# Optimization experiments

Measured on AMD Instinct MI355X. Metric: run time of the kernel, lower is better.

Reference implementation:

```python
import jax, jax.numpy as jnp
import numpy as np

B = 4096          # batch
N_ENT = 200000    # n_entities
N_USR = 50000
N_REL = 32
K = 64            # neighbors per entity
D2 = 128          # dim*2
EPS = 1e-5


def setup_inputs() -> dict:
    key = jax.random.key(0)
    ks = jax.random.split(key, 10)
    return {
        "u": jax.random.randint(ks[0], (B,), 0, N_USR),
        "i": jax.random.randint(ks[1], (B,), 0, N_ENT),
        "adj_entity": jax.random.randint(ks[2], (N_ENT, K), 0, N_ENT),
        "adj_relation": jax.random.randint(ks[3], (N_ENT, K), 0, N_REL),
        "entity_embs": jax.random.normal(ks[4], (N_ENT, D2), jnp.float32),
        "relation_embs": jax.random.normal(ks[5], (N_REL, D2), jnp.float32),
        "bn_gamma": jnp.ones((D2,), jnp.float32),
        "bn_beta": jnp.zeros((D2,), jnp.float32),
        "bn_mean": jnp.zeros((D2,), jnp.float32),
        "bn_var": jnp.ones((D2,), jnp.float32),
        "Wr1_w": jax.random.normal(ks[6], (D2, D2), jnp.float32) * 0.05,
        "Wr1_b": jnp.zeros((D2,), jnp.float32),
        "W1_w": jax.random.normal(ks[7], (D2, D2), jnp.float32) * 0.05,
        "W1_b": jnp.zeros((D2,), jnp.float32),
        "wl_w": jax.random.normal(ks[8], (2 * D2, 1), jnp.float32) * 0.05,
        "wl_b": jnp.zeros((1,), jnp.float32),
    }


def reference(u, i, adj_entity, adj_relation, entity_embs, relation_embs,
              bn_gamma, bn_beta, bn_mean, bn_var,
              Wr1_w, Wr1_b, W1_w, W1_b, wl_w, wl_b):
    # eval mode: all dropout / edge-drop are identity, BN uses running stats
    def bn(x):
        return (x - bn_mean) * bn_gamma * jax.lax.rsqrt(bn_var + EPS) + bn_beta

    def lrelu(x):
        return jnp.where(x >= 0, x, 0.2 * x)

    def layer(h, idx):
        t = entity_embs[adj_entity[idx]]        # [B, K, D2] neighbor gather
        r = relation_embs[adj_relation[idx]]    # [B, K, D2]
        tr = t @ Wr1_w + Wr1_b                  # Wr1(t)
        hr = jnp.tanh((h @ Wr1_w + Wr1_b)[:, None, :] + r)
        hrt = hr * tr                           # [B, K, D2]
        s = jnp.sum(hrt, axis=1)
        Nh = s * s - jnp.sum(hrt * hrt, axis=1)  # FM: sq-of-sum - sum-of-sq
        out = lrelu((h + Nh) @ W1_w + W1_b)      # agg_method='other'
        return h + out

    u_e = bn(entity_embs[u])
    h = bn(entity_embs[i])
    # n_layers = 1
    h = layer(h, i)
    u_e = layer(u_e, u)
    combined = jnp.concatenate([u_e, h], axis=-1)  # [B, 2*D2]
    return (combined @ wl_w + wl_b)[:, 0]
```

## Files before the change

kernel.cpp:

```cpp
#include <hip/hip_runtime.h>

#define B     4096
#define KNB   64
#define D     128
#define NREL  32
#define EPS   1e-5f

typedef __attribute__((ext_vector_type(8))) short bf16x8;
typedef __attribute__((ext_vector_type(4))) float f32x4;

__device__ inline unsigned short f2bf(float f) {
    unsigned u = __float_as_uint(f);
    return (unsigned short)((u + 0x7FFFu + ((u >> 16) & 1u)) >> 16);
}
__device__ inline unsigned cvt_pk_bf16(float lo, float hi) {
    unsigned r;
    asm("v_cvt_pk_bf16_f32 %0, %1, %2" : "=v"(r) : "v"(lo), "v"(hi));
    return r;
}
__device__ inline unsigned short cvt1_bf16(float f) {
    return (unsigned short)(cvt_pk_bf16(f, f) & 0xFFFFu);
}
__device__ inline float bfu_lo(unsigned u) { return __uint_as_float(u << 16); }
__device__ inline float bfu_hi(unsigned u) { return __uint_as_float(u & 0xFFFF0000u); }

__device__ inline float fast_tanh(float x) {
    float e = __builtin_amdgcn_exp2f(x * 2.885390082f);
    return 1.f - 2.f * __builtin_amdgcn_rcpf(e + 1.f);
}

__global__ __launch_bounds__(256) void prep(
    const float* __restrict__ W, unsigned short* __restrict__ Wt,
    const float* __restrict__ gamma, const float* __restrict__ beta,
    const float* __restrict__ mean,  const float* __restrict__ var,
    float* __restrict__ scale, float* __restrict__ shift)
{
    const int t = threadIdx.x;
    const int g = blockIdx.x * 256 + t;
    const int n  = g >> 4;
    const int k0 = (g & 15) * 8;
    unsigned short h[8];
    #pragma unroll
    for (int i = 0; i < 8; ++i) h[i] = f2bf(W[(k0 + i) * D + n]);
    *(uint4*)&Wt[(size_t)n * D + k0] = *(const uint4*)h;

    if (blockIdx.x == 0 && t < D) {
        const float sc = gamma[t] * rsqrtf(var[t] + EPS);
        scale[t] = sc;
        shift[t] = beta[t] - mean[t] * sc;
    }
}

__global__ __launch_bounds__(256) void gemm_etr(
    const float* __restrict__ embs, const unsigned short* __restrict__ Wt,
    const float* __restrict__ bias, unsigned short* __restrict__ outbf,
    const int* __restrict__ i_idx, const int* __restrict__ u_idx,
    const float* __restrict__ scale, const float* __restrict__ shift,
    float* __restrict__ h0out, float* __restrict__ out2, int nb1)
{
    __shared__ unsigned short Al[64 * 128];
    __shared__ unsigned short Wl[128 * 128];

    const int t = threadIdx.x;
    const bool second = (int)blockIdx.x >= nb1;
    const size_t row0 = (size_t)(second ? (int)blockIdx.x - nb1 : (int)blockIdx.x) * 64;

    {
        const float4* w4 = (const float4*)Wt;
        #pragma unroll
        for (int m = 0; m < 8; ++m) {
            const int c = m * 256 + t;
            const int n = c >> 4;
            float4 v = w4[c];
            *(float4*)((char*)Wl + ((c * 16) ^ ((n & 7) << 4))) = v;
        }
    }
    if (!second) {
        #pragma unroll
        for (int m = 0; m < 4; ++m) {
            const int c = m * 256 + t;
            const int r = c >> 4;
            const int k0 = (c & 15) * 8;
            const float4* s = (const float4*)&embs[(row0 + r) * D + k0];
            const float4 x = s[0], y = s[1];
            uint4 h;
            h.x = cvt_pk_bf16(x.x, x.y);
            h.y = cvt_pk_bf16(x.z, x.w);
            h.z = cvt_pk_bf16(y.x, y.y);
            h.w = cvt_pk_bf16(y.z, y.w);
            *(uint4*)((char*)Al + ((r * 256 + k0 * 2) ^ ((r & 7) << 4))) = h;
        }
    } else {
        #pragma unroll
        for (int m = 0; m < 4; ++m) {
            const int c = m * 256 + t;
            const int r = c >> 4;
            const int k0 = (c & 15) * 8;
            const int grow = (int)row0 + r;
            const int bb = grow & (B - 1);
            const int idxv = (grow >= B) ? u_idx[bb] : i_idx[bb];
            const float4* s = (const float4*)&embs[(size_t)idxv * D + k0];
            const float4 x = s[0], y = s[1];
            const float4 sc0 = *(const float4*)&scale[k0];
            const float4 sc1 = *(const float4*)&scale[k0 + 4];
            const float4 sh0 = *(const float4*)&shift[k0];
            const float4 sh1 = *(const float4*)&shift[k0 + 4];
            float4 a0, a1;
            a0.x = fmaf(x.x, sc0.x, sh0.x); a0.y = fmaf(x.y, sc0.y, sh0.y);
            a0.z = fmaf(x.z, sc0.z, sh0.z); a0.w = fmaf(x.w, sc0.w, sh0.w);
            a1.x = fmaf(y.x, sc1.x, sh1.x); a1.y = fmaf(y.y, sc1.y, sh1.y);
            a1.z = fmaf(y.z, sc1.z, sh1.z); a1.w = fmaf(y.w, sc1.w, sh1.w);
            *(float4*)&h0out[(size_t)grow * D + k0]     = a0;
            *(float4*)&h0out[(size_t)grow * D + k0 + 4] = a1;
            uint4 h;
            h.x = cvt_pk_bf16(a0.x, a0.y);
            h.y = cvt_pk_bf16(a0.z, a0.w);
            h.z = cvt_pk_bf16(a1.x, a1.y);
            h.w = cvt_pk_bf16(a1.z, a1.w);
            *(uint4*)((char*)Al + ((r * 256 + k0 * 2) ^ ((r & 7) << 4))) = h;
        }
    }
    __syncthreads();

    const int wv   = t >> 6;
    const int lane = t & 63;
    const int rw   = wv * 16;
    const int lrow = lane & 15;
    const int kgrp = lane >> 4;

    f32x4 acc[8];
    #pragma unroll
    for (int n = 0; n < 8; ++n) acc[n] = (f32x4){0.f, 0.f, 0.f, 0.f};

    #pragma unroll
    for (int ks = 0; ks < 4; ++ks) {
        const int arow = rw + lrow;
        const bf16x8 a = *(const bf16x8*)((const char*)Al +
            ((arow * 256 + ks * 64 + kgrp * 16) ^ ((arow & 7) << 4)));
        #pragma unroll
        for (int n = 0; n < 8; ++n) {
            const int brow = n * 16 + lrow;
            const bf16x8 b = *(const bf16x8*)((const char*)Wl +
                ((brow * 256 + ks * 64 + kgrp * 16) ^ ((brow & 7) << 4)));
            acc[n] = __builtin_amdgcn_mfma_f32_16x16x32_bf16(a, b, acc[n], 0, 0, 0);
        }
    }

    if (second) {
        #pragma unroll
        for (int n = 0; n < 8; ++n) {
            const float bv = bias[n * 16 + lrow];
            #pragma unroll
            for (int i = 0; i < 4; ++i) {
                const size_t r = row0 + rw + kgrp * 4 + i;
                out2[r * D + n * 16 + lrow] = acc[n][i] + bv;
            }
        }
        return;
    }

    __syncthreads();
    #pragma unroll
    for (int n = 0; n < 8; ++n) {
        const float bv = bias[n * 16 + lrow];
        #pragma unroll
        for (int i = 0; i < 4; ++i) {
            const int r = rw + kgrp * 4 + i;
            const int cb = (r * 256 + (n * 16 + lrow) * 2) ^ ((r & 7) << 4);
            *(unsigned short*)((char*)Al + cb) = cvt1_bf16(acc[n][i] + bv);
        }
    }
    __syncthreads();
    {
        float4* dst = (float4*)(outbf + row0 * D);
        #pragma unroll
        for (int m = 0; m < 4; ++m) {
            const int c = m * 256 + t;
            const int r = c >> 4;
            dst[c] = *(const float4*)((const char*)Al + ((c * 16) ^ ((r & 7) << 4)));
        }
    }
}

__global__ __launch_bounds__(256, 8) void aggregate(
    const int* __restrict__ i_idx, const int* __restrict__ u_idx,
    const int* __restrict__ adj_e, const int* __restrict__ adj_r,
    const unsigned short* __restrict__ Etr, const float* __restrict__ rel_embs,
    const float* __restrict__ hW,  const float* __restrict__ h0,
    float* __restrict__ g_out)
{
    __shared__ float tt[NREL * D];
    __shared__ int ents[KNB];
    __shared__ int rels[KNB];
    float* ps = tt;
    float* pq = tt + 4 * D;

    const int t = threadIdx.x;
    const int b = blockIdx.x & (B - 1);
    const int j = blockIdx.x >> 12;
    const size_t rowbase = ((size_t)j * B + b) * D;
    const int idx = j ? u_idx[b] : i_idx[b];

    const float4 hv = *(const float4*)&hW[rowbase + (t & 31) * 4];
    float h0v = 0.f;
    if (t < D) h0v = h0[rowbase + t];

    if (t < KNB) {
        ents[t] = adj_e[(size_t)idx * KNB + t] * (D * 2);
        rels[t] = adj_r[(size_t)idx * KNB + t] * (D * 4);
    }
    __syncthreads();

    const int dq  = t & 31;
    const int grp = t >> 5;
    const char* Eb = (const char*)Etr + dq * 8;
    const char* tb = (const char*)tt  + dq * 16;

    uint2 ev[8];
    #pragma unroll
    for (int it = 0; it < 8; ++it)
        ev[it] = *(const uint2*)(Eb + ents[grp + it * 8]);

    {
        const float4* re4 = (const float4*)rel_embs;
        #pragma unroll
        for (int c = 0; c < 4; ++c) {
            const int m4 = t + c * 256;
            const float4 r = re4[m4];
            float4 o;
            o.x = fast_tanh(hv.x + r.x);
            o.y = fast_tanh(hv.y + r.y);
            o.z = fast_tanh(hv.z + r.z);
            o.w = fast_tanh(hv.w + r.w);
            *(float4*)&tt[m4 * 4] = o;
        }
    }
    __syncthreads();

    float s0 = 0.f, s1 = 0.f, s2 = 0.f, s3 = 0.f;
    float q0 = 0.f, q1 = 0.f, q2 = 0.f, q3 = 0.f;
    #pragma unroll
    for (int it = 0; it < 8; ++it) {
        const float4 tv = *(const float4*)(tb + rels[grp + it * 8]);
        const float v0 = bfu_lo(ev[it].x) * tv.x;
        const float v1 = bfu_hi(ev[it].x) * tv.y;
        const float v2 = bfu_lo(ev[it].y) * tv.z;
        const float v3 = bfu_hi(ev[it].y) * tv.w;
        s0 += v0; s1 += v1; s2 += v2; s3 += v3;
        q0 = fmaf(v0, v0, q0); q1 = fmaf(v1, v1, q1);
        q2 = fmaf(v2, v2, q2); q3 = fmaf(v3, v3, q3);
    }
    s0 += __shfl_xor(s0, 32); s1 += __shfl_xor(s1, 32);
    s2 += __shfl_xor(s2, 32); s3 += __shfl_xor(s3, 32);
    q0 += __shfl_xor(q0, 32); q1 += __shfl_xor(q1, 32);
    q2 += __shfl_xor(q2, 32); q3 += __shfl_xor(q3, 32);

    __syncthreads();

    const int wv = t >> 6;
    if ((t & 63) < 32) {
        *(float4*)&ps[wv * D + dq * 4] = make_float4(s0, s1, s2, s3);
        *(float4*)&pq[wv * D + dq * 4] = make_float4(q0, q1, q2, q3);
    }
    __syncthreads();

    if (t < D) {
        const float ss = ps[t] + ps[D + t] + ps[2 * D + t] + ps[3 * D + t];
        const float qq = pq[t] + pq[D + t] + pq[2 * D + t] + pq[3 * D + t];
        g_out[rowbase + t] = h0v + ss * ss - qq;
    }
}

__global__ __launch_bounds__(256) void gemm_fin(
    const float* __restrict__ gb, const float* __restrict__ W,
    const float* __restrict__ bias, const float* __restrict__ h0,
    const float* __restrict__ wl_w, const float* __restrict__ wl_b,
    float* __restrict__ out)
{
    __shared__ float Wl[64 * 128];
    __shared__ float inl[32 * 128];
    __shared__ float rowdot[32];
    const int t = threadIdx.x;
    const int b0 = blockIdx.x * 16;

    {
        const float4* gb4 = (const float4*)gb;
        float4* inl4 = (float4*)inl;
        #pragma unroll
        for (int m = 0; m < 4; ++m) {
            const int c = m * 256 + t;
            const int r = c >> 5;
            const size_t grow = (r < 16) ? (size_t)(b0 + r) : (size_t)(B + b0 + r - 16);
            inl4[c] = gb4[grow * 32 + (c & 31)];
        }
    }

    const int c0 = (t & 31) * 4;
    const int r0 = (t >> 5) * 4;

    float acc[4][4];
    {
        float4 bv = *(const float4*)&bias[c0];
        #pragma unroll
        for (int i = 0; i < 4; ++i) {
            acc[i][0] = bv.x; acc[i][1] = bv.y; acc[i][2] = bv.z; acc[i][3] = bv.w;
        }
    }

    #pragma unroll
    for (int chunk = 0; chunk < 2; ++chunk) {
        __syncthreads();
        {
            const float4* W4 = (const float4*)(W + chunk * 64 * D);
            float4* Wl4 = (float4*)Wl;
            #pragma unroll
            for (int m = 0; m < 8; ++m) Wl4[t + m * 256] = W4[t + m * 256];
        }
        __syncthreads();
        for (int k = 0; k < 64; k += 4) {
            float4 a[4], w[4];
            #pragma unroll
            for (int i = 0; i < 4; ++i)
                a[i] = *(const float4*)&inl[(r0 + i) * D + chunk * 64 + k];
            #pragma unroll
            for (int kk = 0; kk < 4; ++kk)
                w[kk] = *(const float4*)&Wl[(k + kk) * D + c0];
            #pragma unroll
            for (int i = 0; i < 4; ++i) {
                const float* ai = (const float*)&a[i];
                #pragma unroll
                for (int kk = 0; kk < 4; ++kk) {
                    acc[i][0] = fmaf(ai[kk], w[kk].x, acc[i][0]);
                    acc[i][1] = fmaf(ai[kk], w[kk].y, acc[i][1]);
                    acc[i][2] = fmaf(ai[kk], w[kk].z, acc[i][2]);
                    acc[i][3] = fmaf(ai[kk], w[kk].w, acc[i][3]);
                }
            }
        }
    }

    const int seg = (r0 < 16) ? 128 : 0;
    const float4 wv = *(const float4*)&wl_w[seg + c0];
    float pr[4];
    #pragma unroll
    for (int i = 0; i < 4; ++i) {
        const int r = r0 + i;
        const size_t grow = (r < 16) ? (size_t)(b0 + r) : (size_t)(B + b0 + r - 16);
        const float4 ad = *(const float4*)&h0[grow * D + c0];
        float4 o;
        o.x = ad.x + (acc[i][0] >= 0.f ? acc[i][0] : 0.2f * acc[i][0]);
        o.y = ad.y + (acc[i][1] >= 0.f ? acc[i][1] : 0.2f * acc[i][1]);
        o.z = ad.z + (acc[i][2] >= 0.f ? acc[i][2] : 0.2f * acc[i][2]);
        o.w = ad.w + (acc[i][3] >= 0.f ? acc[i][3] : 0.2f * acc[i][3]);
        pr[i] = o.x * wv.x + o.y * wv.y + o.z * wv.z + o.w * wv.w;
    }
    #pragma unroll
    for (int off = 1; off <= 16; off <<= 1) {
        pr[0] += __shfl_xor(pr[0], off);
        pr[1] += __shfl_xor(pr[1], off);
        pr[2] += __shfl_xor(pr[2], off);
        pr[3] += __shfl_xor(pr[3], off);
    }
    if ((t & 31) == 0) {
        rowdot[r0]     = pr[0];
        rowdot[r0 + 1] = pr[1];
        rowdot[r0 + 2] = pr[2];
        rowdot[r0 + 3] = pr[3];
    }
    __syncthreads();
    if (t < 16) out[b0 + t] = wl_b[0] + rowdot[t + 16] + rowdot[t];
}

extern "C" void kernel_launch(void* const* d_in, const int* in_sizes, int n_in,
                              void* d_out, int out_size, void* d_ws, size_t ws_size,
                              hipStream_t stream) {
    const int*   u        = (const int*)d_in[0];
    const int*   ii       = (const int*)d_in[1];
    const int*   adj_e    = (const int*)d_in[2];
    const int*   adj_r    = (const int*)d_in[3];
    const float* embs     = (const float*)d_in[4];
    const float* rel_embs = (const float*)d_in[5];
    const float* gamma    = (const float*)d_in[6];
    const float* beta     = (const float*)d_in[7];
    const float* mean     = (const float*)d_in[8];
    const float* var      = (const float*)d_in[9];
    const float* Wr1_w    = (const float*)d_in[10];
    const float* Wr1_b    = (const float*)d_in[11];
    const float* W1_w     = (const float*)d_in[12];
    const float* W1_b     = (const float*)d_in[13];
    const float* wl_w     = (const float*)d_in[14];
    const float* wl_b     = (const float*)d_in[15];
    float* out = (float*)d_out;

    const int n_ent = in_sizes[2] / KNB;
    const int nb1 = n_ent / 64;

    char* p = (char*)d_ws;
    unsigned short* Etr = (unsigned short*)p;           p += (size_t)n_ent * D * 2;
    unsigned short* Wt  = (unsigned short*)p;           p += (size_t)D * D * 2;
    float* scale = (float*)p;                           p += D * 4;
    float* shift = (float*)p;                           p += D * 4;
    float* h0   = (float*)p;                            p += (size_t)2 * B * D * 4;
    float* hWb  = (float*)p;                            p += (size_t)2 * B * D * 4;
    float* gb   = (float*)p;

    prep<<<8, 256, 0, stream>>>(Wr1_w, Wt, gamma, beta, mean, var, scale, shift);
    gemm_etr<<<nb1 + (2 * B) / 64, 256, 0, stream>>>(embs, Wt, Wr1_b, Etr,
                                                     ii, u, scale, shift, h0, hWb, nb1);
    aggregate<<<2 * B, 256, 0, stream>>>(ii, u, adj_e, adj_r, Etr, rel_embs, hWb, h0, gb);
    gemm_fin<<<B / 16, 256, 0, stream>>>(gb, W1_w, W1_b, h0, wl_w, wl_b, out);
}
```

Before: 68.57 us.

## Halve aggregate block size, store tanh table as bf16, prescale tanh inputs

New measurement: 142.9 us. 108% more time.

```diff
diff --git a/kernel.cpp b/kernel.cpp
--- a/kernel.cpp
+++ b/kernel.cpp
@@ -5,6 +5,7 @@
 #define D     128
 #define NREL  32
 #define EPS   1e-5f
+#define TSCALE 2.885390082f
 
 typedef __attribute__((ext_vector_type(8))) short bf16x8;
 typedef __attribute__((ext_vector_type(4))) float f32x4;
@@ -24,8 +25,8 @@
 __device__ inline float bfu_lo(unsigned u) { return __uint_as_float(u << 16); }
 __device__ inline float bfu_hi(unsigned u) { return __uint_as_float(u & 0xFFFF0000u); }
 
-__device__ inline float fast_tanh(float x) {
-    float e = __builtin_amdgcn_exp2f(x * 2.885390082f);
+__device__ inline float fast_tanh_ps(float a) {
+    float e = __builtin_amdgcn_exp2f(a);
     return 1.f - 2.f * __builtin_amdgcn_rcpf(e + 1.f);
 }
 
@@ -33,7 +34,8 @@
     const float* __restrict__ W, unsigned short* __restrict__ Wt,
     const float* __restrict__ gamma, const float* __restrict__ beta,
     const float* __restrict__ mean,  const float* __restrict__ var,
-    float* __restrict__ scale, float* __restrict__ shift)
+    float* __restrict__ scale, float* __restrict__ shift,
+    const float* __restrict__ rel_embs, float* __restrict__ re2)
 {
     const int t = threadIdx.x;
     const int g = blockIdx.x * 256 + t;
@@ -44,6 +46,13 @@
     for (int i = 0; i < 8; ++i) h[i] = f2bf(W[(k0 + i) * D + n]);
     *(uint4*)&Wt[(size_t)n * D + k0] = *(const uint4*)h;
 
+    if (blockIdx.x < 2) {
+        #pragma unroll
+        for (int m = 0; m < 8; ++m) {
+            const int i = blockIdx.x * 2048 + m * 256 + t;
+            re2[i] = rel_embs[i] * TSCALE;
+        }
+    }
     if (blockIdx.x == 0 && t < D) {
         const float sc = gamma[t] * rsqrtf(var[t] + EPS);
         scale[t] = sc;
@@ -153,7 +162,7 @@
             #pragma unroll
             for (int i = 0; i < 4; ++i) {
                 const size_t r = row0 + rw + kgrp * 4 + i;
-                out2[r * D + n * 16 + lrow] = acc[n][i] + bv;
+                out2[r * D + n * 16 + lrow] = (acc[n][i] + bv) * TSCALE;
             }
         }
         return;
@@ -182,18 +191,18 @@
     }
 }
 
-__global__ __launch_bounds__(256, 8) void aggregate(
+__global__ __launch_bounds__(128, 8) void aggregate(
     const int* __restrict__ i_idx, const int* __restrict__ u_idx,
     const int* __restrict__ adj_e, const int* __restrict__ adj_r,
-    const unsigned short* __restrict__ Etr, const float* __restrict__ rel_embs,
+    const unsigned short* __restrict__ Etr, const float* __restrict__ re2,
     const float* __restrict__ hW,  const float* __restrict__ h0,
     float* __restrict__ g_out)
 {
-    __shared__ float tt[NREL * D];
+    __shared__ unsigned short tt[NREL * D];
     __shared__ int ents[KNB];
     __shared__ int rels[KNB];
-    float* ps = tt;
-    float* pq = tt + 4 * D;
+    float* ps = (float*)tt;
+    float* pq = (float*)tt + 2 * D;
 
     const int t = threadIdx.x;
     const int b = blockIdx.x & (B - 1);
@@ -201,55 +210,67 @@
     const size_t rowbase = ((size_t)j * B + b) * D;
     const int idx = j ? u_idx[b] : i_idx[b];
 
-    const float4 hv = *(const float4*)&hW[rowbase + (t & 31) * 4];
-    float h0v = 0.f;
-    if (t < D) h0v = h0[rowbase + t];
+    const float2 hv = *(const float2*)&hW[rowbase + 2 * (t & 63)];
+    const float h0v = h0[rowbase + t];
 
     if (t < KNB) {
         ents[t] = adj_e[(size_t)idx * KNB + t] * (D * 2);
-        rels[t] = adj_r[(size_t)idx * KNB + t] * (D * 4);
+        rels[t] = adj_r[(size_t)idx * KNB + t] * (D * 2);
     }
     __syncthreads();
 
     const int dq  = t & 31;
     const int grp = t >> 5;
     const char* Eb = (const char*)Etr + dq * 8;
-    const char* tb = (const char*)tt  + dq * 16;
-
-    uint2 ev[8];
+    const char* tb = (const char*)tt  + dq * 8;
+
+    uint2 ev1[8];
     #pragma unroll
     for (int it = 0; it < 8; ++it)
-        ev[it] = *(const uint2*)(Eb + ents[grp + it * 8]);
-
-    {
-        const float4* re4 = (const float4*)rel_embs;
-        #pragma unroll
-        for (int c = 0; c < 4; ++c) {
-            const int m4 = t + c * 256;
-            const float4 r = re4[m4];
-            float4 o;
-            o.x = fast_tanh(hv.x + r.x);
-            o.y = fast_tanh(hv.y + r.y);
-            o.z = fast_tanh(hv.z + r.z);
-            o.w = fast_tanh(hv.w + r.w);
-            *(float4*)&tt[m4 * 4] = o;
-        }
-    }
+        ev1[it] = *(const uint2*)(Eb + ents[grp + it * 4]);
+
+    {
+        unsigned* tt32 = (unsigned*)tt;
+        #pragma unroll
+        for (int c = 0; c < 16; ++c) {
+            const int q = t + c * 128;
+            const float2 r2 = *(const float2*)&re2[2 * q];
+            const float t0 = fast_tanh_ps(hv.x + r2.x);
+            const float t1 = fast_tanh_ps(hv.y + r2.y);
+            tt32[q] = cvt_pk_bf16(t0, t1);
+        }
+    }
+    uint2 ev2[8];
+    #pragma unroll
+    for (int it = 0; it < 8; ++it)
+        ev2[it] = *(const uint2*)(Eb + ents[grp + 32 + it * 4]);
     __syncthreads();
 
     float s0 = 0.f, s1 = 0.f, s2 = 0.f, s3 = 0.f;
     float q0 = 0.f, q1 = 0.f, q2 = 0.f, q3 = 0.f;
     #pragma unroll
     for (int it = 0; it < 8; ++it) {
-        const float4 tv = *(const float4*)(tb + rels[grp + it * 8]);
-        const float v0 = bfu_lo(ev[it].x) * tv.x;
-        const float v1 = bfu_hi(ev[it].x) * tv.y;
-        const float v2 = bfu_lo(ev[it].y) * tv.z;
-        const float v3 = bfu_hi(ev[it].y) * tv.w;
+        const uint2 tv = *(const uint2*)(tb + rels[grp + it * 4]);
+        const float v0 = bfu_lo(ev1[it].x) * bfu_lo(tv.x);
+        const float v1 = bfu_hi(ev1[it].x) * bfu_hi(tv.x);
+        const float v2 = bfu_lo(ev1[it].y) * bfu_lo(tv.y);
+        const float v3 = bfu_hi(ev1[it].y) * bfu_hi(tv.y);
         s0 += v0; s1 += v1; s2 += v2; s3 += v3;
         q0 = fmaf(v0, v0, q0); q1 = fmaf(v1, v1, q1);
         q2 = fmaf(v2, v2, q2); q3 = fmaf(v3, v3, q3);
     }
+    #pragma unroll
+    for (int it = 0; it < 8; ++it) {
+        const uint2 tv = *(const uint2*)(tb + rels[grp + 32 + it * 4]);
+        const float v0 = bfu_lo(ev2[it].x) * bfu_lo(tv.x);
+        const float v1 = bfu_hi(ev2[it].x) * bfu_hi(tv.x);
+        const float v2 = bfu_lo(ev2[it].y) * bfu_lo(tv.y);
+        const float v3 = bfu_hi(ev2[it].y) * bfu_hi(tv.y);
+        s0 += v0; s1 += v1; s2 += v2; s3 += v3;
+        q0 = fmaf(v0, v0, q0); q1 = fmaf(v1, v1, q1);
+        q2 = fmaf(v2, v2, q2); q3 = fmaf(v3, v3, q3);
+    }
+
     s0 += __shfl_xor(s0, 32); s1 += __shfl_xor(s1, 32);
     s2 += __shfl_xor(s2, 32); s3 += __shfl_xor(s3, 32);
     q0 += __shfl_xor(q0, 32); q1 += __shfl_xor(q1, 32);
@@ -264,9 +285,9 @@
     }
     __syncthreads();
 
-    if (t < D) {
-        const float ss = ps[t] + ps[D + t] + ps[2 * D + t] + ps[3 * D + t];
-        const float qq = pq[t] + pq[D + t] + pq[2 * D + t] + pq[3 * D + t];
+    {
+        const float ss = ps[t] + ps[D + t];
+        const float qq = pq[t] + pq[D + t];
         g_out[rowbase + t] = h0v + ss * ss - qq;
     }
 }
@@ -400,13 +421,15 @@
     unsigned short* Wt  = (unsigned short*)p;           p += (size_t)D * D * 2;
     float* scale = (float*)p;                           p += D * 4;
     float* shift = (float*)p;                           p += D * 4;
+    float* re2   = (float*)p;                           p += (size_t)NREL * D * 4;
     float* h0   = (float*)p;                            p += (size_t)2 * B * D * 4;
     float* hWb  = (float*)p;                            p += (size_t)2 * B * D * 4;
     float* gb   = (float*)p;
 
-    prep<<<8, 256, 0, stream>>>(Wr1_w, Wt, gamma, beta, mean, var, scale, shift);
+    prep<<<8, 256, 0, stream>>>(Wr1_w, Wt, gamma, beta, mean, var, scale, shift,
+                                rel_embs, re2);
     gemm_etr<<<nb1 + (2 * B) / 64, 256, 0, stream>>>(embs, Wt, Wr1_b, Etr,
                                                      ii, u, scale, shift, h0, hWb, nb1);
-    aggregate<<<2 * B, 256, 0, stream>>>(ii, u, adj_e, adj_r, Etr, rel_embs, hWb, h0, gb);
+    aggregate<<<2 * B, 128, 0, stream>>>(ii, u, adj_e, adj_r, Etr, re2, hWb, h0, gb);
     gemm_fin<<<B / 16, 256, 0, stream>>>(gb, W1_w, W1_b, h0, wl_w, wl_b, out);
 }
```
